# Optimization experiments

Hardware: AMD Instinct MI355X
Metric: run time of the kernel (lower is better)

Reference implementation:

```python
import jax, jax.numpy as jnp
import numpy as np

NUM_PROTEINS = 19000
NUM_DRUGS = 4000
NUM_CELL_LINES = 16
BATCH = 4096
NUM_EDGES = 40000
LAYERS = [2048, 1024, 1]
IN_DIM = 2 * (NUM_PROTEINS + NUM_CELL_LINES)  # 38032


def setup_inputs() -> dict:
    key = jax.random.key(0)
    ks = jax.random.split(key, 10)
    inp = {
        "drug_pairs": jax.random.randint(ks[0], (BATCH, 2), 0, NUM_DRUGS, dtype=jnp.int64 if jax.config.jax_enable_x64 else jnp.int32),
        "cell_lines": jax.random.randint(ks[1], (BATCH,), 0, NUM_CELL_LINES),
        "dpi_drug": jax.random.randint(ks[2], (NUM_EDGES,), 0, NUM_DRUGS),
        "dpi_prot": jax.random.randint(ks[3], (NUM_EDGES,), 0, NUM_PROTEINS),
        "W0": jax.random.normal(ks[4], (LAYERS[0], IN_DIM), dtype=jnp.float32) * 0.02,
        "b0": jnp.zeros((LAYERS[0],), dtype=jnp.float32),
        "W1": jax.random.normal(ks[5], (LAYERS[1], LAYERS[0]), dtype=jnp.float32) * 0.02,
        "b1": jnp.zeros((LAYERS[1],), dtype=jnp.float32),
        "W2": jax.random.normal(ks[6], (LAYERS[2], LAYERS[1]), dtype=jnp.float32) * 0.02,
        "b2": jnp.zeros((LAYERS[2],), dtype=jnp.float32),
    }
    return inp


def _mlp(x, W0, b0, W1, b1, W2, b2):
    h = jax.nn.relu(x @ W0.T + b0)
    h = jax.nn.relu(h @ W1.T + b1)
    return h @ W2.T + b2


def reference(drug_pairs, cell_lines, dpi_drug, dpi_prot, W0, b0, W1, b1, W2, b2):
    # Build drug -> protein multi-hot table with a single vectorized scatter
    # (replaces the per-row Python loop: prot[i, targets] = 1)
    table = jnp.zeros((NUM_DRUGS, NUM_PROTEINS), dtype=jnp.float32)
    table = table.at[dpi_drug, dpi_prot].set(1.0)

    prot_1 = table[drug_pairs[:, 0]]  # [B, P]
    prot_2 = table[drug_pairs[:, 1]]  # [B, P]
    one_hot_cl = jax.nn.one_hot(cell_lines, NUM_CELL_LINES, dtype=jnp.float32)  # [B, C]

    bd1 = jnp.concatenate([prot_1, one_hot_cl], axis=1)
    bd2 = jnp.concatenate([prot_2, one_hot_cl], axis=1)
    x1 = jnp.concatenate([bd1, bd2], axis=1)  # [B, 2*(P+C)]
    x2 = jnp.concatenate([bd2, bd1], axis=1)

    out1 = _mlp(x1, W0, b0, W1, b1, W2, b2)
    out2 = _mlp(x2, W0, b0, W1, b1, W2, b2)
    return (out1[:, 0], out2[:, 0])
```

## Files before the change

### kernel.cpp

```cpp
#include <hip/hip_runtime.h>
#include <hip/hip_bf16.h>
#include <stdint.h>

#define NPROT 19000
#define NDRUG 4000
#define NCELL 16
#define BATCH 4096
#define NEDGE 40000
#define L0 2048
#define L1DIM 1024
#define INDIM 38032
#define HALFDIM 19016
#define WSTN 19008
#define DCAP 96
#define BMWORDS ((NDRUG * NPROT + 31) / 32)
#define NQUAD 512

typedef float f32x4 __attribute__((ext_vector_type(4)));
typedef short s16x8 __attribute__((ext_vector_type(8)));

__global__ void zero_all_kernel(int* __restrict__ p, int n) {
    int i = blockIdx.x * 256 + threadIdx.x;
    if (i < n) p[i] = 0;
}

__global__ void scatter_dedup_kernel(const int* __restrict__ drug, const int* __restrict__ prot,
                                     unsigned* __restrict__ bitmap, int* __restrict__ cnt,
                                     unsigned short* __restrict__ dlist) {
    int e = blockIdx.x * 256 + threadIdx.x;
    if (e < NEDGE) {
        int d = drug[e], p = prot[e];
        unsigned idx = (unsigned)d * NPROT + p;
        unsigned bit = 1u << (idx & 31u);
        unsigned old = atomicOr(&bitmap[idx >> 5], bit);
        if (!(old & bit)) {
            int pos = atomicAdd(&cnt[d], 1);
            if (pos < DCAP) dlist[d * DCAP + pos] = (unsigned short)p;
        }
    }
}

__global__ __launch_bounds__(512) void stream_meta_kernel(const int* __restrict__ cnt,
                                                          int* __restrict__ wlen,
                                                          int* __restrict__ wbase,
                                                          int* __restrict__ pref,
                                                          int* __restrict__ tcnt) {
    __shared__ int wl[8];
    int t = threadIdx.x;
    if (t < 8) wl[t] = 0;
    __syncthreads();
    int c = 0;
#pragma unroll
    for (int k = 0; k < 8; ++k) {
        int d = t + (k << 9);
        pref[t * 8 + k] = c;
        if (d < NDRUG) c += max(min(cnt[d], DCAP), 1);
    }
    tcnt[t] = c;
    atomicMax(&wl[t >> 6], c);
    __syncthreads();
    if (t == 0) {
        int run = 0;
        for (int w = 0; w < 8; ++w) {
            wlen[w] = wl[w];
            wbase[w] = run;
            run += wl[w] * 64;
        }
    }
}

__global__ __launch_bounds__(256) void fill_stream_kernel(const int* __restrict__ cnt,
                                                          const unsigned short* __restrict__ dlist,
                                                          const int* __restrict__ wbase,
                                                          const int* __restrict__ wlen,
                                                          const int* __restrict__ pref,
                                                          const int* __restrict__ tcnt,
                                                          unsigned short* __restrict__ estream) {
    int g = blockIdx.x * 256 + threadIdx.x;
    if (g < NDRUG) {
        int d = g;
        int t = d & 511, k = d >> 9;
        int base = wbase[t >> 6] + (t & 63);
        int idx = pref[t * 8 + k];
        int n = min(cnt[d], DCAP);
        if (n == 0) {
            estream[base + idx * 64] = (unsigned short)(19000 | 0x8000);
        } else {
            for (int i = 0; i < n; ++i) {
                unsigned short e = dlist[d * DCAP + i];
                if (i == n - 1) e |= 0x8000;
                estream[base + (idx + i) * 64] = e;
            }
        }
    } else if (g < NDRUG + 512) {
        int t = g - NDRUG;
        int base = wbase[t >> 6] + (t & 63);
        int wl = wlen[t >> 6];
        for (int idx = tcnt[t]; idx < wl; ++idx)
            estream[base + idx * 64] = (unsigned short)19000;
    }
}

__global__ void base_kernel(const float* __restrict__ W0, const float* __restrict__ b0,
                            float* __restrict__ BASE) {
    int i = blockIdx.x * 256 + threadIdx.x;
    if (i < NCELL * L0) {
        int c = i >> 11, ch = i & 2047;
        const float* wr = W0 + (size_t)ch * INDIM;
        BASE[(size_t)c * L0 + ch] = b0[ch] + wr[NPROT + c] + wr[HALFDIM + NPROT + c];
    }
}

__device__ inline unsigned bfpair(float a, float b) {
    unsigned ua = __float_as_uint(a), ub = __float_as_uint(b);
    ua += 0x7fffu + ((ua >> 16) & 1u);
    ub += 0x7fffu + ((ub >> 16) & 1u);
    return (ua >> 16) | (ub & 0xffff0000u);
}
__device__ inline float bflo(unsigned w) { return __uint_as_float(w << 16); }
__device__ inline float bfhi(unsigned w) { return __uint_as_float(w & 0xffff0000u); }

__global__ __launch_bounds__(512) void drug_sum_kernel(const float* __restrict__ W0,
                                                       const unsigned short* __restrict__ estream,
                                                       const int* __restrict__ wbase,
                                                       const int* __restrict__ wlen,
                                                       uint2* __restrict__ SAT,
                                                       uint2* __restrict__ SBT) {
    __shared__ uint2 wst[WSTN];
    int t = threadIdx.x;
    int bid = blockIdx.x;
    int hb = bid >> 9;
    int k2 = bid & 511;
    int ch0 = k2 * 4;
    size_t colbase = (size_t)hb * HALFDIM;

    int wv = t >> 6;
    int base = wbase[wv] + (t & 63);
    int wl = wlen[wv];
    int nfull = wl >> 3, rem = wl & 7;
    unsigned e[8];
    if (nfull > 0) {
#pragma unroll
        for (int k = 0; k < 8; ++k) e[k] = estream[base + k * 64];
        base += 512;
    }

    const float* sA = W0 + (size_t)(ch0 + 0) * INDIM + colbase;
    const float* sB = W0 + (size_t)(ch0 + 1) * INDIM + colbase;
    const float* sC = W0 + (size_t)(ch0 + 2) * INDIM + colbase;
    const float* sD = W0 + (size_t)(ch0 + 3) * INDIM + colbase;
#pragma unroll
    for (int k = 0; k < 9; ++k) {
        int i = t * 4 + k * 2048;
        float4 a = *(const float4*)(sA + i);
        float4 b = *(const float4*)(sB + i);
        float4 c = *(const float4*)(sC + i);
        float4 d = *(const float4*)(sD + i);
        uint4 q0, q1;
        q0.x = bfpair(a.x, b.x); q0.y = bfpair(c.x, d.x);
        q0.z = bfpair(a.y, b.y); q0.w = bfpair(c.y, d.y);
        q1.x = bfpair(a.z, b.z); q1.y = bfpair(c.z, d.z);
        q1.z = bfpair(a.w, b.w); q1.w = bfpair(c.w, d.w);
        *(uint4*)&wst[i] = q0;
        *(uint4*)&wst[i + 2] = q1;
    }
    {
        int i = t * 4 + 9 * 2048;
        if (i < 19000) {
            float4 a = *(const float4*)(sA + i);
            float4 b = *(const float4*)(sB + i);
            float4 c = *(const float4*)(sC + i);
            float4 d = *(const float4*)(sD + i);
            uint4 q0, q1;
            q0.x = bfpair(a.x, b.x); q0.y = bfpair(c.x, d.x);
            q0.z = bfpair(a.y, b.y); q0.w = bfpair(c.y, d.y);
            q1.x = bfpair(a.z, b.z); q1.y = bfpair(c.z, d.z);
            q1.z = bfpair(a.w, b.w); q1.w = bfpair(c.w, d.w);
            *(uint4*)&wst[i] = q0;
            *(uint4*)&wst[i + 2] = q1;
        }
    }
    if (t < 8) { wst[19000 + t].x = 0u; wst[19000 + t].y = 0u; }
    __syncthreads();

    float x0 = 0.f, x1 = 0.f, x2 = 0.f, x3 = 0.f;
    int kk = 0;
    uint2* dstT = (hb ? SBT : SAT) + (size_t)k2 * NDRUG;

    auto process = [&](const unsigned* ev) {
#pragma unroll
        for (int k = 0; k < 8; ++k) {
            uint2 w = wst[ev[k] & 0x7fffu];
            x0 += bflo(w.x);
            x1 += bfhi(w.x);
            x2 += bflo(w.y);
            x3 += bfhi(w.y);
            if (ev[k] & 0x8000u) {
                uint2 v;
                v.x = bfpair(x0, x1);
                v.y = bfpair(x2, x3);
                dstT[t + (kk << 9)] = v;
                ++kk; x0 = 0.f; x1 = 0.f; x2 = 0.f; x3 = 0.f;
            }
        }
    };

    if (nfull > 0) {
        for (int it = 1; it < nfull; ++it) {
            unsigned f[8];
#pragma unroll
            for (int k = 0; k < 8; ++k) f[k] = estream[base + k * 64];
            base += 512;
            process(e);
#pragma unroll
            for (int k = 0; k < 8; ++k) e[k] = f[k];
        }
        process(e);
    }
    for (int k = 0; k < rem; ++k) {
        unsigned ev = estream[base + k * 64];
        uint2 w = wst[ev & 0x7fffu];
        x0 += bflo(w.x);
        x1 += bfhi(w.x);
        x2 += bflo(w.y);
        x3 += bfhi(w.y);
        if (ev & 0x8000u) {
            uint2 v;
            v.x = bfpair(x0, x1);
            v.y = bfpair(x2, x3);
            dstT[t + (kk << 9)] = v;
            ++kk; x0 = 0.f; x1 = 0.f; x2 = 0.f; x3 = 0.f;
        }
    }
}

__global__ __launch_bounds__(256) void transpose_kernel(const uint2* __restrict__ SAT,
                                                        const uint2* __restrict__ SBT,
                                                        uint2* __restrict__ SAb,
                                                        uint2* __restrict__ SBb) {
    __shared__ uint2 tile[32][33];
    const int KT = NQUAD / 32;
    const int DT = NDRUG / 32;
    int b = blockIdx.x;
    int half = b / (KT * DT);
    int rem = b % (KT * DT);
    int k0 = (rem / DT) * 32;
    int d0 = (rem % DT) * 32;
    const uint2* in = half ? SBT : SAT;
    uint2* out = half ? SBb : SAb;
    int tx = threadIdx.x & 31, ty = threadIdx.x >> 5;
#pragma unroll
    for (int r = 0; r < 32; r += 8)
        tile[r + ty][tx] = in[(size_t)(k0 + r + ty) * NDRUG + d0 + tx];
    __syncthreads();
#pragma unroll
    for (int r = 0; r < 32; r += 8)
        out[(size_t)(d0 + r + ty) * NQUAD + k0 + tx] = tile[tx][r + ty];
}

__global__ void cvtw1_kernel(const float* __restrict__ W1, __hip_bfloat16* __restrict__ W1b) {
    int i = blockIdx.x * 256 + threadIdx.x;
    const int n = L1DIM * L0 / 4;
    if (i < n) {
        float4 v = ((const float4*)W1)[i];
        uint2 q;
        q.x = bfpair(v.x, v.y);
        q.y = bfpair(v.z, v.w);
        ((uint2*)W1b)[i] = q;
    }
}

__global__ __launch_bounds__(256) void build_h_kernel(const int* __restrict__ dp,
                                                      const int* __restrict__ cl,
                                                      const __hip_bfloat16* __restrict__ SAb,
                                                      const __hip_bfloat16* __restrict__ SBb,
                                                      const float* __restrict__ BASE,
                                                      __hip_bfloat16* __restrict__ h1) {
    int b = blockIdx.x;
    int d1 = dp[2 * b], d2 = dp[2 * b + 1], c = cl[b];
    int ch = threadIdx.x * 8;
    const float* bs = BASE + (size_t)c * L0 + ch;
    uint4 ua1 = *(const uint4*)(SAb + (size_t)d1 * L0 + ch);
    uint4 ua2 = *(const uint4*)(SAb + (size_t)d2 * L0 + ch);
    uint4 us1 = *(const uint4*)(SBb + (size_t)d1 * L0 + ch);
    uint4 us2 = *(const uint4*)(SBb + (size_t)d2 * L0 + ch);
    float4 vb0 = *(const float4*)(bs);
    float4 vb1 = *(const float4*)(bs + 4);
    float bsv[8] = {vb0.x, vb0.y, vb0.z, vb0.w, vb1.x, vb1.y, vb1.z, vb1.w};
    unsigned a1w[4] = {ua1.x, ua1.y, ua1.z, ua1.w};
    unsigned a2w[4] = {ua2.x, ua2.y, ua2.z, ua2.w};
    unsigned s1w[4] = {us1.x, us1.y, us1.z, us1.w};
    unsigned s2w[4] = {us2.x, us2.y, us2.z, us2.w};
    float z1[8], z2[8];
#pragma unroll
    for (int k = 0; k < 4; ++k) {
        z1[2 * k]     = fmaxf(bsv[2 * k]     + bflo(a1w[k]) + bflo(s2w[k]), 0.f);
        z1[2 * k + 1] = fmaxf(bsv[2 * k + 1] + bfhi(a1w[k]) + bfhi(s2w[k]), 0.f);
        z2[2 * k]     = fmaxf(bsv[2 * k]     + bflo(a2w[k]) + bflo(s1w[k]), 0.f);
        z2[2 * k + 1] = fmaxf(bsv[2 * k + 1] + bfhi(a2w[k]) + bfhi(s1w[k]), 0.f);
    }
    uint4 o1, o2;
    o1.x = bfpair(z1[0], z1[1]); o1.y = bfpair(z1[2], z1[3]);
    o1.z = bfpair(z1[4], z1[5]); o1.w = bfpair(z1[6], z1[7]);
    o2.x = bfpair(z2[0], z2[1]); o2.y = bfpair(z2[2], z2[3]);
    o2.z = bfpair(z2[4], z2[5]); o2.w = bfpair(z2[6], z2[7]);
    *(uint4*)((__hip_bfloat16*)h1 + (size_t)b * L0 + ch) = o1;
    *(uint4*)((__hip_bfloat16*)h1 + (size_t)(BATCH + b) * L0 + ch) = o2;
}

__global__ void init_out_kernel(float* __restrict__ out, const float* __restrict__ b2, int n) {
    int i = blockIdx.x * 256 + threadIdx.x;
    if (i < n) out[i] = b2[0];
}

#define BM 128
#define BN 128
#define BK2 64
__global__ __launch_bounds__(256) void gemm_kernel(const __hip_bfloat16* __restrict__ A,
                                                   const __hip_bfloat16* __restrict__ B,
                                                   const float* __restrict__ bias,
                                                   const float* __restrict__ W2,
                                                   float* __restrict__ out,
                                                   int M, int N, int K) {
    __shared__ __hip_bfloat16 As[BM * BK2];
    __shared__ __hip_bfloat16 Bs[BN * BK2];
    int t = threadIdx.x;
    int bid = blockIdx.x;
    int xcd = bid & 7, ii2 = bid >> 3;
    int by = xcd * 8 + (ii2 >> 3);
    int bx = ii2 & 7;
    int brow = by * BM, bcol = bx * BN;
    int w = t >> 6, l = t & 63;
    int wr = w >> 1, wc = w & 1;
    f32x4 acc[4][4] = {};
    int row = l & 15, ko = (l >> 4) * 8;
    int swz = (row & 7) * 8;
    for (int k0 = 0; k0 < K; k0 += BK2) {
#pragma unroll
        for (int i = 0; i < 4; ++i) {
            int idx = i * 256 + t;
            int r = idx >> 3;
            int cb = ((idx & 7) ^ (r & 7)) * 8;
            __builtin_amdgcn_global_load_lds(
                (const __attribute__((address_space(1))) void*)(A + (size_t)(brow + r) * K + k0 + cb),
                (__attribute__((address_space(3))) void*)(&As[idx * 8]), 16, 0, 0);
            __builtin_amdgcn_global_load_lds(
                (const __attribute__((address_space(1))) void*)(B + (size_t)(bcol + r) * K + k0 + cb),
                (__attribute__((address_space(3))) void*)(&Bs[idx * 8]), 16, 0, 0);
        }
        __syncthreads();
#pragma unroll
        for (int ks = 0; ks < 2; ++ks) {
            int col = (ks * 32 + ko) ^ swz;
            s16x8 af[4], bfr[4];
#pragma unroll
            for (int m = 0; m < 4; ++m)
                af[m] = *(const s16x8*)(&As[(wr * 64 + m * 16 + row) * BK2 + col]);
#pragma unroll
            for (int n = 0; n < 4; ++n)
                bfr[n] = *(const s16x8*)(&Bs[(wc * 64 + n * 16 + row) * BK2 + col]);
#pragma unroll
            for (int m = 0; m < 4; ++m)
#pragma unroll
                for (int n = 0; n < 4; ++n)
                    acc[m][n] = __builtin_amdgcn_mfma_f32_16x16x32_bf16(af[m], bfr[n], acc[m][n], 0, 0, 0);
        }
        __syncthreads();
    }
    int cr = (l >> 4) * 4;
    int cc = l & 15;
#pragma unroll
    for (int m = 0; m < 4; ++m) {
        float s[4] = {0.f, 0.f, 0.f, 0.f};
#pragma unroll
        for (int n = 0; n < 4; ++n) {
            int gcol = bcol + wc * 64 + n * 16 + cc;
            float bv = bias[gcol];
            float wv = W2[gcol];
#pragma unroll
            for (int j = 0; j < 4; ++j) {
                float v = fmaxf(acc[m][n][j] + bv, 0.f);
                s[j] += v * wv;
            }
        }
#pragma unroll
        for (int mask = 1; mask < 16; mask <<= 1) {
#pragma unroll
            for (int j = 0; j < 4; ++j) s[j] += __shfl_xor(s[j], mask);
        }
        if (cc == 0) {
            int grow = brow + wr * 64 + m * 16 + cr;
#pragma unroll
            for (int j = 0; j < 4; ++j) atomicAdd(&out[grow + j], s[j]);
        }
    }
}

extern "C" void kernel_launch(void* const* d_in, const int* in_sizes, int n_in,
                              void* d_out, int out_size, void* d_ws, size_t ws_size,
                              hipStream_t stream) {
    const int* drug_pairs = (const int*)d_in[0];
    const int* cell_lines = (const int*)d_in[1];
    const int* dpi_drug = (const int*)d_in[2];
    const int* dpi_prot = (const int*)d_in[3];
    const float* W0 = (const float*)d_in[4];
    const float* b0 = (const float*)d_in[5];
    const float* W1 = (const float*)d_in[6];
    const float* b1 = (const float*)d_in[7];
    const float* W2 = (const float*)d_in[8];
    const float* b2 = (const float*)d_in[9];
    float* out = (float*)d_out;

    char* ws = (char*)d_ws;
    size_t off = 0;
    auto alloc = [&](size_t bytes) {
        char* p = ws + off;
        off += (bytes + 255) & ~(size_t)255;
        return p;
    };
    __hip_bfloat16* SAb = (__hip_bfloat16*)alloc((size_t)NDRUG * L0 * 2);
    __hip_bfloat16* SBb = (__hip_bfloat16*)alloc((size_t)NDRUG * L0 * 2);
    uint2* SAT = (uint2*)alloc((size_t)NQUAD * NDRUG * 8);
    uint2* SBT = (uint2*)alloc((size_t)NQUAD * NDRUG * 8);
    float* BASE = (float*)alloc((size_t)NCELL * L0 * 4);
    __hip_bfloat16* W1b = (__hip_bfloat16*)alloc((size_t)L1DIM * L0 * 2);
    __hip_bfloat16* h1 = (__hip_bfloat16*)alloc((size_t)2 * BATCH * L0 * 2);
    const int ZREG_N = BMWORDS + NDRUG;
    int* zreg = (int*)alloc((size_t)ZREG_N * 4);
    unsigned* bitmap = (unsigned*)zreg;
    int* cnt = zreg + BMWORDS;
    unsigned short* dlist = (unsigned short*)alloc((size_t)NDRUG * DCAP * 2);
    int* wlen = (int*)alloc(8 * 4);
    int* wbase = (int*)alloc(8 * 4);
    int* pref = (int*)alloc((size_t)512 * 8 * 4);
    int* tcnt = (int*)alloc((size_t)512 * 4);
    unsigned short* estream = (unsigned short*)alloc((size_t)64 * (NEDGE + NDRUG + 512) * 2);

    zero_all_kernel<<<(ZREG_N + 255) / 256, 256, 0, stream>>>(zreg, ZREG_N);
    scatter_dedup_kernel<<<(NEDGE + 255) / 256, 256, 0, stream>>>(dpi_drug, dpi_prot,
                                                                  bitmap, cnt, dlist);
    stream_meta_kernel<<<1, 512, 0, stream>>>(cnt, wlen, wbase, pref, tcnt);
    fill_stream_kernel<<<(NDRUG + 512 + 255) / 256, 256, 0, stream>>>(cnt, dlist, wbase,
                                                                      wlen, pref, tcnt, estream);
    base_kernel<<<(NCELL * L0 + 255) / 256, 256, 0, stream>>>(W0, b0, BASE);
    drug_sum_kernel<<<2 * NQUAD, 512, 0, stream>>>(W0, estream, wbase, wlen, SAT, SBT);
    transpose_kernel<<<2 * (NQUAD / 32) * (NDRUG / 32), 256, 0, stream>>>(SAT, SBT,
                                                                          (uint2*)SAb, (uint2*)SBb);
    cvtw1_kernel<<<(L1DIM * L0 / 4 + 255) / 256, 256, 0, stream>>>(W1, W1b);
    build_h_kernel<<<BATCH, 256, 0, stream>>>(drug_pairs, cell_lines, SAb, SBb, BASE, h1);
    init_out_kernel<<<(2 * BATCH + 255) / 256, 256, 0, stream>>>(out, b2, 2 * BATCH);
    gemm_kernel<<<(2 * BATCH / BM) * (L1DIM / BN), 256, 0, stream>>>(h1, W1b, b1, W2, out,
                                                                     2 * BATCH, L1DIM, L0);
}
```

Measured before the change: 228.9 us.

## Split protein range in half to shrink LDS table and double drug-sum blocks

The drug-sum kernel now splits the protein axis into two halves, so each block stages only about 9.5K bf16 weight quads in shared memory instead of 19K. That halves LDS use per block and doubles the grid, which should raise occupancy and parallelism. Partial sums are written as fp32 float4 and added by a new combine kernel that also transposes and converts to bf16, replacing the old transpose. The cost is a much larger fp32 intermediate buffer (128MB) with more global write and read traffic, plus extra per-half counting and padding in the edge streams.

```diff
diff --git a/kernel.cpp b/kernel.cpp
--- a/kernel.cpp
+++ b/kernel.cpp
@@ -11,10 +11,11 @@
 #define L1DIM 1024
 #define INDIM 38032
 #define HALFDIM 19016
-#define WSTN 19008
 #define DCAP 96
 #define BMWORDS ((NDRUG * NPROT + 31) / 32)
-#define NQUAD 512
+#define PSPLIT 9504
+#define WSLOT 9504
+#define WSTN2 9512
 
 typedef float f32x4 __attribute__((ext_vector_type(4)));
 typedef short s16x8 __attribute__((ext_vector_type(8)));
@@ -25,8 +26,8 @@
 }
 
 __global__ void scatter_dedup_kernel(const int* __restrict__ drug, const int* __restrict__ prot,
-                                     unsigned* __restrict__ bitmap, int* __restrict__ cnt,
-                                     unsigned short* __restrict__ dlist) {
+                                     unsigned* __restrict__ bitmap, int* __restrict__ cnt2,
+                                     int* __restrict__ cntTot, unsigned short* __restrict__ dlist) {
     int e = blockIdx.x * 256 + threadIdx.x;
     if (e < NEDGE) {
         int d = drug[e], p = prot[e];
@@ -34,42 +35,51 @@
         unsigned bit = 1u << (idx & 31u);
         unsigned old = atomicOr(&bitmap[idx >> 5], bit);
         if (!(old & bit)) {
-            int pos = atomicAdd(&cnt[d], 1);
+            int ph = p >= PSPLIT;
+            atomicAdd(&cnt2[d * 2 + ph], 1);
+            int pos = atomicAdd(&cntTot[d], 1);
             if (pos < DCAP) dlist[d * DCAP + pos] = (unsigned short)p;
         }
     }
 }
 
-__global__ __launch_bounds__(512) void stream_meta_kernel(const int* __restrict__ cnt,
+__global__ __launch_bounds__(512) void stream_meta_kernel(const int* __restrict__ cnt2,
                                                           int* __restrict__ wlen,
                                                           int* __restrict__ wbase,
                                                           int* __restrict__ pref,
                                                           int* __restrict__ tcnt) {
-    __shared__ int wl[8];
+    __shared__ int wl[16];
     int t = threadIdx.x;
-    if (t < 8) wl[t] = 0;
+    if (t < 16) wl[t] = 0;
     __syncthreads();
-    int c = 0;
+    int c0 = 0, c1 = 0;
 #pragma unroll
     for (int k = 0; k < 8; ++k) {
         int d = t + (k << 9);
-        pref[t * 8 + k] = c;
-        if (d < NDRUG) c += max(min(cnt[d], DCAP), 1);
-    }
-    tcnt[t] = c;
-    atomicMax(&wl[t >> 6], c);
+        pref[((t << 3) + k) * 2 + 0] = c0;
+        pref[((t << 3) + k) * 2 + 1] = c1;
+        if (d < NDRUG) {
+            int n0 = cnt2[d * 2], n1 = cnt2[d * 2 + 1];
+            c0 += n0 ? n0 : 1;
+            c1 += n1 ? n1 : 1;
+        }
+    }
+    tcnt[t * 2] = c0;
+    tcnt[t * 2 + 1] = c1;
+    atomicMax(&wl[(t >> 6) * 2], c0);
+    atomicMax(&wl[(t >> 6) * 2 + 1], c1);
     __syncthreads();
     if (t == 0) {
         int run = 0;
-        for (int w = 0; w < 8; ++w) {
-            wlen[w] = wl[w];
-            wbase[w] = run;
-            run += wl[w] * 64;
-        }
-    }
-}
-
-__global__ __launch_bounds__(256) void fill_stream_kernel(const int* __restrict__ cnt,
+        for (int s = 0; s < 16; ++s) {
+            wlen[s] = wl[s];
+            wbase[s] = run;
+            run += wl[s] * 64;
+        }
+    }
+}
+
+__global__ __launch_bounds__(256) void fill_stream_kernel(const int* __restrict__ cnt2,
                                                           const unsigned short* __restrict__ dlist,
                                                           const int* __restrict__ wbase,
                                                           const int* __restrict__ wlen,
@@ -80,24 +90,36 @@
     if (g < NDRUG) {
         int d = g;
         int t = d & 511, k = d >> 9;
-        int base = wbase[t >> 6] + (t & 63);
-        int idx = pref[t * 8 + k];
-        int n = min(cnt[d], DCAP);
-        if (n == 0) {
-            estream[base + idx * 64] = (unsigned short)(19000 | 0x8000);
-        } else {
-            for (int i = 0; i < n; ++i) {
-                unsigned short e = dlist[d * DCAP + i];
-                if (i == n - 1) e |= 0x8000;
-                estream[base + (idx + i) * 64] = e;
+        int wv = t >> 6, lane = t & 63;
+        int n0 = cnt2[d * 2], n1 = cnt2[d * 2 + 1];
+        int base0 = wbase[wv * 2 + 0] + lane;
+        int base1 = wbase[wv * 2 + 1] + lane;
+        int i0 = pref[((t << 3) + k) * 2 + 0];
+        int i1 = pref[((t << 3) + k) * 2 + 1];
+        int n = min(n0 + n1, DCAP);
+        int j0 = 0, j1 = 0;
+        for (int i = 0; i < n; ++i) {
+            int p = dlist[d * DCAP + i];
+            if (p < PSPLIT) {
+                unsigned short e = (unsigned short)(p | ((j0 == n0 - 1) ? 0x8000 : 0));
+                estream[base0 + (i0 + j0) * 64] = e;
+                ++j0;
+            } else {
+                unsigned short e = (unsigned short)((p - PSPLIT) | ((j1 == n1 - 1) ? 0x8000 : 0));
+                estream[base1 + (i1 + j1) * 64] = e;
+                ++j1;
             }
         }
-    } else if (g < NDRUG + 512) {
-        int t = g - NDRUG;
-        int base = wbase[t >> 6] + (t & 63);
-        int wl = wlen[t >> 6];
-        for (int idx = tcnt[t]; idx < wl; ++idx)
-            estream[base + idx * 64] = (unsigned short)19000;
+        if (n0 == 0) estream[base0 + i0 * 64] = (unsigned short)(WSLOT | 0x8000);
+        if (n1 == 0) estream[base1 + i1 * 64] = (unsigned short)(WSLOT | 0x8000);
+    } else if (g < NDRUG + 1024) {
+        int idx = g - NDRUG;
+        int t = idx >> 1, ph = idx & 1;
+        int wv = t >> 6;
+        int base = wbase[wv * 2 + ph] + (t & 63);
+        int wl = wlen[wv * 2 + ph];
+        for (int j = tcnt[t * 2 + ph]; j < wl; ++j)
+            estream[base + j * 64] = (unsigned short)WSLOT;
     }
 }
 
@@ -124,19 +146,22 @@
                                                        const unsigned short* __restrict__ estream,
                                                        const int* __restrict__ wbase,
                                                        const int* __restrict__ wlen,
-                                                       uint2* __restrict__ SAT,
-                                                       uint2* __restrict__ SBT) {
-    __shared__ uint2 wst[WSTN];
+                                                       float4* __restrict__ SAT) {
+    __shared__ uint2 wst[WSTN2];
     int t = threadIdx.x;
     int bid = blockIdx.x;
-    int hb = bid >> 9;
-    int k2 = bid & 511;
-    int ch0 = k2 * 4;
-    size_t colbase = (size_t)hb * HALFDIM;
+    int ph = bid >> 10;
+    int k3 = bid & 1023;
+    int hb = k3 >> 9;
+    int quad = k3 & 511;
+    int ch0 = quad * 4;
+    size_t colbase = (size_t)hb * HALFDIM + (size_t)ph * PSPLIT;
+    int pc = ph ? (NPROT - PSPLIT) : PSPLIT;
 
     int wv = t >> 6;
-    int base = wbase[wv] + (t & 63);
-    int wl = wlen[wv];
+    int sid = wv * 2 + ph;
+    int base = wbase[sid] + (t & 63);
+    int wl = wlen[sid];
     int nfull = wl >> 3, rem = wl & 7;
     unsigned e[8];
     if (nfull > 0) {
@@ -150,7 +175,7 @@
     const float* sC = W0 + (size_t)(ch0 + 2) * INDIM + colbase;
     const float* sD = W0 + (size_t)(ch0 + 3) * INDIM + colbase;
 #pragma unroll
-    for (int k = 0; k < 9; ++k) {
+    for (int k = 0; k < 4; ++k) {
         int i = t * 4 + k * 2048;
         float4 a = *(const float4*)(sA + i);
         float4 b = *(const float4*)(sB + i);
@@ -165,8 +190,8 @@
         *(uint4*)&wst[i + 2] = q1;
     }
     {
-        int i = t * 4 + 9 * 2048;
-        if (i < 19000) {
+        int i = t * 4 + 8192;
+        if (i < pc) {
             float4 a = *(const float4*)(sA + i);
             float4 b = *(const float4*)(sB + i);
             float4 c = *(const float4*)(sC + i);
@@ -180,82 +205,80 @@
             *(uint4*)&wst[i + 2] = q1;
         }
     }
-    if (t < 8) { wst[19000 + t].x = 0u; wst[19000 + t].y = 0u; }
+    if (t < 8) { wst[WSLOT + t].x = 0u; wst[WSLOT + t].y = 0u; }
     __syncthreads();
 
     float x0 = 0.f, x1 = 0.f, x2 = 0.f, x3 = 0.f;
     int kk = 0;
-    uint2* dstT = (hb ? SBT : SAT) + (size_t)k2 * NDRUG;
-
-    auto process = [&](const unsigned* ev) {
-#pragma unroll
-        for (int k = 0; k < 8; ++k) {
-            uint2 w = wst[ev[k] & 0x7fffu];
-            x0 += bflo(w.x);
-            x1 += bfhi(w.x);
-            x2 += bflo(w.y);
-            x3 += bfhi(w.y);
-            if (ev[k] & 0x8000u) {
-                uint2 v;
-                v.x = bfpair(x0, x1);
-                v.y = bfpair(x2, x3);
-                dstT[t + (kk << 9)] = v;
-                ++kk; x0 = 0.f; x1 = 0.f; x2 = 0.f; x3 = 0.f;
-            }
-        }
-    };
-
-    if (nfull > 0) {
-        for (int it = 1; it < nfull; ++it) {
-            unsigned f[8];
-#pragma unroll
-            for (int k = 0; k < 8; ++k) f[k] = estream[base + k * 64];
-            base += 512;
-            process(e);
-#pragma unroll
-            for (int k = 0; k < 8; ++k) e[k] = f[k];
-        }
-        process(e);
-    }
-    for (int k = 0; k < rem; ++k) {
-        unsigned ev = estream[base + k * 64];
+    float4* dstT = SAT + (size_t)bid * 4096;
+
+    auto proc = [&](unsigned ev) {
         uint2 w = wst[ev & 0x7fffu];
         x0 += bflo(w.x);
         x1 += bfhi(w.x);
         x2 += bflo(w.y);
         x3 += bfhi(w.y);
         if (ev & 0x8000u) {
-            uint2 v;
-            v.x = bfpair(x0, x1);
-            v.y = bfpair(x2, x3);
+            float4 v;
+            v.x = x0; v.y = x1; v.z = x2; v.w = x3;
             dstT[t + (kk << 9)] = v;
             ++kk; x0 = 0.f; x1 = 0.f; x2 = 0.f; x3 = 0.f;
         }
-    }
-}
-
-__global__ __launch_bounds__(256) void transpose_kernel(const uint2* __restrict__ SAT,
-                                                        const uint2* __restrict__ SBT,
-                                                        uint2* __restrict__ SAb,
-                                                        uint2* __restrict__ SBb) {
-    __shared__ uint2 tile[32][33];
-    const int KT = NQUAD / 32;
-    const int DT = NDRUG / 32;
+    };
+
+    if (nfull > 0) {
+        for (int it = 1; it < nfull; ++it) {
+            unsigned f[8];
+#pragma unroll
+            for (int k = 0; k < 8; ++k) f[k] = estream[base + k * 64];
+            base += 512;
+#pragma unroll
+            for (int k = 0; k < 8; ++k) proc(e[k]);
+#pragma unroll
+            for (int k = 0; k < 8; ++k) e[k] = f[k];
+        }
+#pragma unroll
+        for (int k = 0; k < 8; ++k) proc(e[k]);
+    }
+    for (int k = 0; k < rem; ++k) proc(estream[base + k * 64]);
+}
+
+__global__ __launch_bounds__(256) void combine_kernel(const float4* __restrict__ SAT,
+                                                      __hip_bfloat16* __restrict__ SAb,
+                                                      __hip_bfloat16* __restrict__ SBb) {
+    __shared__ float tile[4][32][33];
     int b = blockIdx.x;
-    int half = b / (KT * DT);
-    int rem = b % (KT * DT);
-    int k0 = (rem / DT) * 32;
-    int d0 = (rem % DT) * 32;
-    const uint2* in = half ? SBT : SAT;
-    uint2* out = half ? SBb : SAb;
+    int hb = b / 2000;
+    int rem = b % 2000;
+    int q0 = (rem / 125) * 32;
+    int d0 = (rem % 125) * 32;
+    const float4* inA = SAT + (size_t)(hb * 512) * 4096;
+    const float4* inB = SAT + (size_t)(1024 + hb * 512) * 4096;
     int tx = threadIdx.x & 31, ty = threadIdx.x >> 5;
 #pragma unroll
-    for (int r = 0; r < 32; r += 8)
-        tile[r + ty][tx] = in[(size_t)(k0 + r + ty) * NDRUG + d0 + tx];
+    for (int r = 0; r < 32; r += 8) {
+        int q = q0 + r + ty;
+        float4 a = inA[(size_t)q * 4096 + d0 + tx];
+        float4 c = inB[(size_t)q * 4096 + d0 + tx];
+        tile[0][r + ty][tx] = a.x + c.x;
+        tile[1][r + ty][tx] = a.y + c.y;
+        tile[2][r + ty][tx] = a.z + c.z;
+        tile[3][r + ty][tx] = a.w + c.w;
+    }
     __syncthreads();
-#pragma unroll
-    for (int r = 0; r < 32; r += 8)
-        out[(size_t)(d0 + r + ty) * NQUAD + k0 + tx] = tile[tx][r + ty];
+    __hip_bfloat16* out = hb ? SBb : SAb;
+#pragma unroll
+    for (int r = 0; r < 32; r += 8) {
+        int d = d0 + r + ty;
+        float x = tile[0][tx][r + ty];
+        float y = tile[1][tx][r + ty];
+        float z = tile[2][tx][r + ty];
+        float w = tile[3][tx][r + ty];
+        uint2 v;
+        v.x = bfpair(x, y);
+        v.y = bfpair(z, w);
+        *(uint2*)(out + (size_t)d * L0 + (q0 + tx) * 4) = v;
+    }
 }
 
 __global__ void cvtw1_kernel(const float* __restrict__ W1, __hip_bfloat16* __restrict__ W1b) {
@@ -420,32 +443,31 @@
     };
     __hip_bfloat16* SAb = (__hip_bfloat16*)alloc((size_t)NDRUG * L0 * 2);
     __hip_bfloat16* SBb = (__hip_bfloat16*)alloc((size_t)NDRUG * L0 * 2);
-    uint2* SAT = (uint2*)alloc((size_t)NQUAD * NDRUG * 8);
-    uint2* SBT = (uint2*)alloc((size_t)NQUAD * NDRUG * 8);
+    float4* SAT = (float4*)alloc((size_t)2048 * 4096 * 16);
     float* BASE = (float*)alloc((size_t)NCELL * L0 * 4);
     __hip_bfloat16* W1b = (__hip_bfloat16*)alloc((size_t)L1DIM * L0 * 2);
     __hip_bfloat16* h1 = (__hip_bfloat16*)alloc((size_t)2 * BATCH * L0 * 2);
-    const int ZREG_N = BMWORDS + NDRUG;
+    const int ZREG_N = BMWORDS + 3 * NDRUG;
     int* zreg = (int*)alloc((size_t)ZREG_N * 4);
     unsigned* bitmap = (unsigned*)zreg;
-    int* cnt = zreg + BMWORDS;
+    int* cnt2 = zreg + BMWORDS;
+    int* cntTot = zreg + BMWORDS + 2 * NDRUG;
     unsigned short* dlist = (unsigned short*)alloc((size_t)NDRUG * DCAP * 2);
-    int* wlen = (int*)alloc(8 * 4);
-    int* wbase = (int*)alloc(8 * 4);
-    int* pref = (int*)alloc((size_t)512 * 8 * 4);
-    int* tcnt = (int*)alloc((size_t)512 * 4);
-    unsigned short* estream = (unsigned short*)alloc((size_t)64 * (NEDGE + NDRUG + 512) * 2);
+    int* wlen = (int*)alloc(16 * 4);
+    int* wbase = (int*)alloc(16 * 4);
+    int* pref = (int*)alloc((size_t)512 * 8 * 2 * 4);
+    int* tcnt = (int*)alloc((size_t)512 * 2 * 4);
+    unsigned short* estream = (unsigned short*)alloc((size_t)64 * (NEDGE + 2 * NDRUG + 2048) * 2);
 
     zero_all_kernel<<<(ZREG_N + 255) / 256, 256, 0, stream>>>(zreg, ZREG_N);
     scatter_dedup_kernel<<<(NEDGE + 255) / 256, 256, 0, stream>>>(dpi_drug, dpi_prot,
-                                                                  bitmap, cnt, dlist);
-    stream_meta_kernel<<<1, 512, 0, stream>>>(cnt, wlen, wbase, pref, tcnt);
-    fill_stream_kernel<<<(NDRUG + 512 + 255) / 256, 256, 0, stream>>>(cnt, dlist, wbase,
-                                                                      wlen, pref, tcnt, estream);
+                                                                  bitmap, cnt2, cntTot, dlist);
+    stream_meta_kernel<<<1, 512, 0, stream>>>(cnt2, wlen, wbase, pref, tcnt);
+    fill_stream_kernel<<<(NDRUG + 1024 + 255) / 256, 256, 0, stream>>>(cnt2, dlist, wbase,
+                                                                       wlen, pref, tcnt, estream);
     base_kernel<<<(NCELL * L0 + 255) / 256, 256, 0, stream>>>(W0, b0, BASE);
-    drug_sum_kernel<<<2 * NQUAD, 512, 0, stream>>>(W0, estream, wbase, wlen, SAT, SBT);
-    transpose_kernel<<<2 * (NQUAD / 32) * (NDRUG / 32), 256, 0, stream>>>(SAT, SBT,
-                                                                          (uint2*)SAb, (uint2*)SBb);
+    drug_sum_kernel<<<2048, 512, 0, stream>>>(W0, estream, wbase, wlen, SAT);
+    combine_kernel<<<4000, 256, 0, stream>>>(SAT, SAb, SBb);
     cvtw1_kernel<<<(L1DIM * L0 / 4 + 255) / 256, 256, 0, stream>>>(W1, W1b);
     build_h_kernel<<<BATCH, 256, 0, stream>>>(drug_pairs, cell_lines, SAb, SBb, BASE, h1);
     init_out_kernel<<<(2 * BATCH + 255) / 256, 256, 0, stream>>>(out, b2, 2 * BATCH);
```

Measured after the change: 237.3 us. +3.7%, slower.
